# Performance work log

Hardware: AMD Instinct MI355X
Metric: run time of the kernel (lower is better)

Reference implementation:

```python
import jax, jax.numpy as jnp
import numpy as np

KEEP_ID, DEL_ID, PAD_ID, STOP_ID, ANNO_ID = 1, 2, 0, 102, 103
V, E, H = 21128, 768, 768
B, T = 8, 256
S = T + 1  # org/simp length; S = T+1 guarantees counters never go out of range


def setup_inputs() -> dict:
    key = jax.random.key(0)
    ks = jax.random.split(key, 16)
    def p(i, shape, scale):
        return jax.random.normal(ks[i], shape, jnp.float32) * scale
    return {
        "input_edits": jax.random.randint(ks[0], (B, T), 0, V),
        "org_ids": jax.random.randint(ks[1], (B, S), 0, V),
        "simp_sent": jax.random.randint(ks[2], (B, S), 0, V),
        "h0": jax.random.normal(ks[3], (B, H), jnp.float32),
        "c0": jax.random.normal(ks[4], (B, H), jnp.float32),
        "encoder_outputs_org": jax.random.normal(ks[5], (B, S, E), jnp.float32),
        "emb": p(6, (V, E), 0.02),
        "Wih_e": p(7, (4 * H, E), 0.03), "Whh_e": p(8, (4 * H, H), 0.03), "b_e": jnp.zeros((4 * H,), jnp.float32),
        "Wih_w": p(9, (4 * H, E), 0.03), "Whh_w": p(10, (4 * H, H), 0.03), "b_w": jnp.zeros((4 * H,), jnp.float32),
        "W_attn": p(11, (H, H), 0.03),
        "W_align": p(12, (H, E), 0.03),
        "W_mlp": p(13, (E, 4 * H), 0.03), "b_mlp": jnp.zeros((E,), jnp.float32),
        "W_out": p(14, (V, E), 0.02), "b_out": jnp.zeros((V,), jnp.float32),
    }


def lstm(x, h0, c0, Wih, Whh, b):
    # x: [B,T,E]; single-layer batch_first LSTM, torch gate order (i,f,g,o)
    def step(carry, xt):
        h, c = carry
        g = xt @ Wih.T + h @ Whh.T + b
        i, f, gg, o = jnp.split(g, 4, axis=-1)
        c2 = jax.nn.sigmoid(f) * c + jax.nn.sigmoid(i) * jnp.tanh(gg)
        h2 = jax.nn.sigmoid(o) * jnp.tanh(c2)
        return (h2, c2), h2
    (hT, cT), hs = jax.lax.scan(step, (h0, c0), jnp.swapaxes(x, 0, 1))
    return jnp.swapaxes(hs, 0, 1), hT, cT


def reference(input_edits, org_ids, simp_sent, h0, c0, encoder_outputs_org,
              emb, Wih_e, Whh_e, b_e, Wih_w, Whh_w, b_w,
              W_attn, W_align, W_mlp, b_mlp, W_out, b_out):
    bsz, nsteps = input_edits.shape
    enc = jnp.tanh(encoder_outputs_org @ W_align.T)            # [B,S,H]
    out_edits, hT, cT = lstm(emb[input_edits], h0, c0, Wih_e, Whh_e, b_e)  # [B,T,H]
    out_words, _, _ = lstm(emb[simp_sent], h0, c0, Wih_w, Whh_w, b_w)      # [B,S,H]

    key = out_edits @ W_attn.T                                  # [B,T,H]
    attn = jax.nn.softmax(jnp.einsum('bth,bsh->bts', key, enc), axis=-1)
    ctx = jnp.einsum('bts,bsh->bth', attn, enc)                 # [B,T,H]

    # counter recurrence (pre-update counters are used for the gathers at step t)
    gold = jnp.swapaxes(input_edits[:, 1:], 0, 1)               # [T-1, B]
    bidx = jnp.arange(bsz)

    def cstep(carry, a):
        kd, ki, an = carry
        kd2 = kd + ((a == KEEP_ID) | (a == DEL_ID)).astype(kd.dtype)
        not_special = (a != DEL_ID) & (a != STOP_ID) & (a != PAD_ID)
        ki2 = ki + not_special.astype(ki.dtype)
        is_ins = not_special & (a != KEEP_ID)
        next_is_anno = org_ids[bidx, an + 1] == ANNO_ID
        an2 = jnp.where(is_ins & next_is_anno, an + 1, jnp.maximum(kd2, an))
        return (kd2, ki2, an2), (ki, an)

    z = jnp.zeros((bsz,), jnp.int32)
    _, (ki_seq, an_seq) = jax.lax.scan(cstep, (z, z, z), gold)
    ki_bt = jnp.swapaxes(ki_seq, 0, 1)                          # [B,T-1]
    an_bt = jnp.swapaxes(an_seq, 0, 1)                          # [B,T-1]

    c = jnp.take_along_axis(enc, an_bt[:, :, None], axis=1)        # [B,T-1,H]
    c_word = jnp.take_along_axis(out_words, ki_bt[:, :, None], axis=1)  # [B,T-1,H]

    Tm1 = nsteps - 1
    feat = jnp.concatenate([out_edits[:, :Tm1], ctx[:, :Tm1], c, c_word], axis=-1)  # [B,T-1,4H]
    mlp = jnp.tanh(feat @ W_mlp.T + b_mlp)                      # [B,T-1,E]
    logp = jax.nn.log_softmax(mlp @ W_out.T + b_out, axis=-1)   # [B,T-1,V]
    return logp, hT, cT
```

## Files before the change

kernel.cpp:

```cpp
#include <hip/hip_runtime.h>
#include <hip/hip_bf16.h>

typedef short s16x8 __attribute__((ext_vector_type(8)));
typedef float f32x4 __attribute__((ext_vector_type(4)));
typedef unsigned short u16;
typedef unsigned short u16x4 __attribute__((ext_vector_type(4)));
typedef unsigned long long u64;
typedef unsigned long long u64x2 __attribute__((ext_vector_type(2)));

__device__ __forceinline__ u16 f2bf(float f) {
  __hip_bfloat16 h = __float2bfloat16(f);
  u16 u;
  __builtin_memcpy(&u, &h, sizeof(u));
  return u;
}
__device__ __forceinline__ float bf2f(u16 u) {
  unsigned int x = ((unsigned int)u) << 16;
  float f;
  __builtin_memcpy(&f, &x, 4);
  return f;
}

__device__ __forceinline__ unsigned int a_ld32(const unsigned int* p) {
  return __hip_atomic_load(p, __ATOMIC_RELAXED, __HIP_MEMORY_SCOPE_AGENT);
}
__device__ __forceinline__ u64 a_ld64(const u64* p) {
  return __hip_atomic_load(p, __ATOMIC_RELAXED, __HIP_MEMORY_SCOPE_AGENT);
}
__device__ __forceinline__ void a_st32(unsigned int* p, unsigned int v) {
  __hip_atomic_store(p, v, __ATOMIC_RELAXED, __HIP_MEMORY_SCOPE_AGENT);
}

__device__ __forceinline__ void gload16(const void* g, void* l) {
  __builtin_amdgcn_global_load_lds(
      (const __attribute__((address_space(1))) unsigned int*)g,
      (__attribute__((address_space(3))) unsigned int*)l, 16, 0, 0);
}

template<int CBF16, int GATHER, int TANHA, int BIAS>
__global__ __launch_bounds__(256) void gemm_bt(
    const u16* __restrict__ A, const u16* __restrict__ B,
    const float* __restrict__ bias, void* __restrict__ Cv,
    const int* __restrict__ ids,
    int M, int N, int K, int lda, int ldb, int ldc,
    long sAz, long sBz, long sCz, int rpb, long cbs)
{
  __shared__ u16 sA[4096];
  __shared__ u16 sB[4096];
  const int tid = threadIdx.x;
  const int z = blockIdx.z;
  const int m0 = blockIdx.y * 128, n0 = blockIdx.x * 128;
  const u16* Ab = A + z * sAz;
  const u16* Bb = B + z * sBz;
  const int w = tid >> 6, lane = tid & 63;
  const int wr = w >> 1, wc = w & 1;
  const int lr = lane & 15, lk = lane >> 4;
  f32x4 acc[4][4] = {};
  const int e0 = tid * 8, e1 = e0 + 2048;
  const int r0 = e0 >> 5, c0 = e0 & 31;
  const int r1 = e1 >> 5, c1 = e1 & 31;
  long arow0, arow1;
  if (GATHER) {
    int i0 = m0 + r0; if (i0 >= M) i0 = M - 1;
    int i1 = m0 + r1; if (i1 >= M) i1 = M - 1;
    arow0 = (long)ids[i0] * lda;
    arow1 = (long)ids[i1] * lda;
  } else {
    arow0 = (long)(m0 + r0) * lda;
    arow1 = (long)(m0 + r1) * lda;
  }
  const long brow0 = (long)(n0 + r0) * ldb;
  const long brow1 = (long)(n0 + r1) * ldb;
  char* sAc = (char*)sA;
  char* sBc = (char*)sB;
  const size_t cb = (size_t)w * 1024;
  for (int kt = 0; kt < K; kt += 32) {
    __syncthreads();
    gload16(Ab + arow0 + kt + c0, sAc + cb);
    gload16(Ab + arow1 + kt + c1, sAc + 4096 + cb);
    gload16(Bb + brow0 + kt + c0, sBc + cb);
    gload16(Bb + brow1 + kt + c1, sBc + 4096 + cb);
    __syncthreads();
    s16x8 af[4], bf[4];
#pragma unroll
    for (int i = 0; i < 4; i++) {
      af[i] = *(const s16x8*)&sA[(wr*64 + i*16 + lr)*32 + lk*8];
      bf[i] = *(const s16x8*)&sB[(wc*64 + i*16 + lr)*32 + lk*8];
    }
#pragma unroll
    for (int mi = 0; mi < 4; mi++)
#pragma unroll
      for (int ni = 0; ni < 4; ni++)
        acc[mi][ni] = __builtin_amdgcn_mfma_f32_16x16x32_bf16(af[mi], bf[ni], acc[mi][ni], 0, 0, 0);
  }
#pragma unroll
  for (int mi = 0; mi < 4; mi++) {
#pragma unroll
    for (int ni = 0; ni < 4; ni++) {
#pragma unroll
      for (int r = 0; r < 4; r++) {
        int gm = m0 + wr*64 + mi*16 + lk*4 + r;
        int gn = n0 + wc*64 + ni*16 + lr;
        if (gm < M && gn < N) {
          float v = acc[mi][ni][r];
          if (BIAS) v += bias[gn];
          if (TANHA) v = tanhf(v);
          long ci = z * sCz + (long)(gm / rpb) * cbs + (long)(gm % rpb) * ldc + gn;
          if (CBF16) ((u16*)Cv)[ci] = f2bf(v);
          else       ((float*)Cv)[ci] = v;
        }
      }
    }
  }
}

__global__ __launch_bounds__(256) void cast_all(
    const float* __restrict__ emb, u16* __restrict__ emb_bf,
    const float* __restrict__ Wout, u16* __restrict__ Wout_bf,
    const float* __restrict__ Wihe, u16* __restrict__ Wihe_bf,
    const float* __restrict__ Wihw, u16* __restrict__ Wihw_bf,
    const float* __restrict__ Wmlp, u16* __restrict__ Wmlp_bf,
    const float* __restrict__ Walign, u16* __restrict__ Walign_bf,
    const float* __restrict__ Wattn, u16* __restrict__ Wattn_bf,
    const float* __restrict__ encoder, u16* __restrict__ encd_bf)
{
  int r = blockIdx.x;
  const float* src; u16* dst; int srows, cols;
  if (r < 21128)                    { src=emb;    dst=emb_bf;    srows=21128; cols=768; }
  else if ((r -= 21128) < 21248)    { src=Wout;   dst=Wout_bf;   srows=21128; cols=768; }
  else if ((r -= 21248) < 3072)     { src=Wihe;   dst=Wihe_bf;   srows=3072;  cols=768; }
  else if ((r -= 3072) < 3072)      { src=Wihw;   dst=Wihw_bf;   srows=3072;  cols=768; }
  else if ((r -= 3072) < 768)       { src=Wmlp;   dst=Wmlp_bf;   srows=768;   cols=3072; }
  else if ((r -= 768) < 768)        { src=Walign; dst=Walign_bf; srows=768;   cols=768; }
  else if ((r -= 768) < 768)        { src=Wattn;  dst=Wattn_bf;  srows=768;   cols=768; }
  else { r -= 768;                    src=encoder; dst=encd_bf;  srows=2056;  cols=768; }
  for (int c = threadIdx.x; c < cols; c += 256) {
    float v = (r < srows) ? src[(long)r * cols + c] : 0.f;
    dst[(long)r * cols + c] = f2bf(v);
  }
}

__global__ void counters_k(const int* __restrict__ input_edits,
                           const int* __restrict__ org_ids,
                           int* __restrict__ ki_bt, int* __restrict__ an_bt,
                           unsigned int* __restrict__ tags)
{
  int b = threadIdx.x;
  for (int i = b; i < 128; i += 64) tags[i] = 0;
  if (b >= 8) return;
  int kd = 0, ki = 0, an = 0;
  for (int t = 0; t < 255; t++) {
    int a = input_edits[b * 256 + t + 1];
    ki_bt[b * 255 + t] = ki;
    an_bt[b * 255 + t] = an;
    int kd2 = kd + ((a == 1) || (a == 2) ? 1 : 0);
    int ns = (a != 2) && (a != 102) && (a != 0);
    int ki2 = ki + (ns ? 1 : 0);
    int is_ins = ns && (a != 1);
    int nia = (org_ids[b * 257 + an + 1] == 103);
    int mx = (kd2 > an) ? kd2 : an;
    int an2 = (is_ins && nia) ? (an + 1) : mx;
    kd = kd2; ki = ki2; an = an2;
  }
}

__global__ __launch_bounds__(256, 1) void lstm_persist(
    const float* __restrict__ Whh_e, const float* __restrict__ Whh_w,
    const float* __restrict__ xW_e, const float* __restrict__ xW_w,
    const float* __restrict__ h0, const float* __restrict__ c0,
    u16* __restrict__ hglob, unsigned int* __restrict__ tags,
    u16* __restrict__ out_e, u16* __restrict__ out_w,
    float* __restrict__ out_tail)
{
  const int wg = blockIdx.x;
  const int l = wg / 24, grp = wg % 24;
  const int u0 = grp * 32;
  const int tid = threadIdx.x;
  const int w = tid >> 6, lane = tid & 63;
  const int c16 = lane & 15, half = lane >> 4;
  const int uh = w >> 1, g0 = (w & 1) * 2;

  __shared__ u16 ldsh[12288];
  __shared__ float Gbuf[16][4][2][16];

  s16x8 wfrag[2][24];
  {
    const float* Wbase = l ? Whh_w : Whh_e;
#pragma unroll
    for (int g = 0; g < 2; g++) {
      const float* Wsrc = Wbase + (long)((g0 + g) * 768 + u0 + uh * 16 + c16) * 768 + half * 8;
#pragma unroll
      for (int s = 0; s < 24; s++) {
        float4 f0 = *(const float4*)(Wsrc + s * 32);
        float4 f1 = *(const float4*)(Wsrc + s * 32 + 4);
        s16x8 v;
        v[0]=f2bf(f0.x); v[1]=f2bf(f0.y); v[2]=f2bf(f0.z); v[3]=f2bf(f0.w);
        v[4]=f2bf(f1.x); v[5]=f2bf(f1.y); v[6]=f2bf(f1.z); v[7]=f2bf(f1.w);
        wfrag[g][s] = v;
      }
    }
  }

  const int ub = tid >> 4, j2 = (tid & 15) * 2;
  const int uA = u0 + j2;
  float creg0 = 0.f, creg1 = 0.f;
  if (tid < 128) {
    creg0 = c0[ub * 768 + uA];
    creg1 = c0[ub * 768 + uA + 1];
  }

  u16* hg = hglob + l * 24576;
  unsigned int* tg = tags + l * 64;
  const int swA = uA ^ ((ub & 7) << 3);

  if (tid < 128) {
    float v0 = h0[ub * 768 + uA], v1 = h0[ub * 768 + uA + 1];
    u16 h0a = f2bf(v0), h0b = f2bf(v1);
    u16 l0a = f2bf(v0 - bf2f(h0a)), l0b = f2bf(v1 - bf2f(h0b));
    a_st32((unsigned int*)&hg[ub * 768 + swA],
           (unsigned int)h0a | ((unsigned int)h0b << 16));
    a_st32((unsigned int*)&hg[(ub + 8) * 768 + swA],
           (unsigned int)l0a | ((unsigned int)l0b << 16));
  }
  __syncthreads();
  if (tid == 0) a_st32(&tg[grp], 1u);

  const int trow = l ? 257 : 256;
  const float* xrb = (l ? xW_w : xW_e) + ((long)ub * trow) * 3072 + uA;
  u16* outp = (l ? out_w : out_e) + (long)ub * 256 * 768 + uA;
  float2 xq0, xq1, xq2, xq3;
  if (tid < 128) {
    xq0 = *(const float2*)&xrb[0];
    xq1 = *(const float2*)&xrb[768];
    xq2 = *(const float2*)&xrb[1536];
    xq3 = *(const float2*)&xrb[2304];
  }

  for (int t = 0; t < 256; t++) {
    float2 nx0, nx1, nx2, nx3;
    if (tid < 128) {
      const float* xn = xrb + (long)(t + 1) * 3072;
      nx0 = *(const float2*)&xn[0];
      nx1 = *(const float2*)&xn[768];
      nx2 = *(const float2*)&xn[1536];
      nx3 = *(const float2*)&xn[2304];
    }

    {
      const unsigned int tgt = (unsigned int)(t + 1);
      const unsigned int* tp = tg + (t & 1) * 32;
      const bool need = (lane < 24) && (lane != grp);
      while (true) {
        unsigned int v = need ? a_ld32(&tp[lane]) : tgt;
        if (!__any(v < tgt)) break;
        __builtin_amdgcn_s_sleep(1);
      }
      asm volatile("" ::: "memory");
    }

    {
      const u64* hs8 = (const u64*)(hg + (t & 1) * 12288);
#pragma unroll
      for (int i = 0; i < 6; i++) {
        const int idx = i * 256 + tid;
        u64 a = a_ld64(&hs8[idx * 2 + 0]);
        u64 b = a_ld64(&hs8[idx * 2 + 1]);
        u64x2 vv; vv[0] = a; vv[1] = b;
        *(u64x2*)&ldsh[idx * 8] = vv;
      }
    }
    __syncthreads();

    f32x4 acc0 = {}, acc1 = {};
#pragma unroll
    for (int s = 0; s < 24; s++) {
      const int off = (c16 * 768 + s * 32 + half * 8) ^ ((c16 & 7) << 3);
      s16x8 a = *(const s16x8*)&ldsh[off];
      acc0 = __builtin_amdgcn_mfma_f32_16x16x32_bf16(a, wfrag[0][s], acc0, 0, 0, 0);
      acc1 = __builtin_amdgcn_mfma_f32_16x16x32_bf16(a, wfrag[1][s], acc1, 0, 0, 0);
    }
#pragma unroll
    for (int r = 0; r < 4; r++) {
      Gbuf[half * 4 + r][g0 + 0][uh][c16] = acc0[r];
      Gbuf[half * 4 + r][g0 + 1][uh][c16] = acc1[r];
    }
    __syncthreads();

    if (tid < 128) {
      const int uh0 = j2 >> 4, uc0 = j2 & 15;
      const int uc1 = (j2 + 1) & 15;
      float gi0 = Gbuf[ub][0][uh0][uc0] + Gbuf[ub + 8][0][uh0][uc0] + xq0.x;
      float gf0 = Gbuf[ub][1][uh0][uc0] + Gbuf[ub + 8][1][uh0][uc0] + xq1.x;
      float gg0 = Gbuf[ub][2][uh0][uc0] + Gbuf[ub + 8][2][uh0][uc0] + xq2.x;
      float go0 = Gbuf[ub][3][uh0][uc0] + Gbuf[ub + 8][3][uh0][uc0] + xq3.x;
      float gi1 = Gbuf[ub][0][uh0][uc1] + Gbuf[ub + 8][0][uh0][uc1] + xq0.y;
      float gf1 = Gbuf[ub][1][uh0][uc1] + Gbuf[ub + 8][1][uh0][uc1] + xq1.y;
      float gg1 = Gbuf[ub][2][uh0][uc1] + Gbuf[ub + 8][2][uh0][uc1] + xq2.y;
      float go1 = Gbuf[ub][3][uh0][uc1] + Gbuf[ub + 8][3][uh0][uc1] + xq3.y;
      float si0 = 1.f / (1.f + expf(-gi0)), si1 = 1.f / (1.f + expf(-gi1));
      float sf0 = 1.f / (1.f + expf(-gf0)), sf1 = 1.f / (1.f + expf(-gf1));
      float so0 = 1.f / (1.f + expf(-go0)), so1 = 1.f / (1.f + expf(-go1));
      float c20 = sf0 * creg0 + si0 * tanhf(gg0);
      float c21 = sf1 * creg1 + si1 * tanhf(gg1);
      float h20 = so0 * tanhf(c20);
      float h21 = so1 * tanhf(c21);
      creg0 = c20; creg1 = c21;
      u16 hiA = f2bf(h20), hiB = f2bf(h21);
      u16 loA = f2bf(h20 - bf2f(hiA)), loB = f2bf(h21 - bf2f(hiB));
      unsigned int hip = (unsigned int)hiA | ((unsigned int)hiB << 16);
      unsigned int lop = (unsigned int)loA | ((unsigned int)loB << 16);
      u16* hb = hg + ((t + 1) & 1) * 12288;
      a_st32((unsigned int*)&hb[ub * 768 + swA], hip);
      a_st32((unsigned int*)&hb[(ub + 8) * 768 + swA], lop);
      *(unsigned int*)&outp[(long)t * 768] = hip;
      if (l == 0 && t == 255) {
        *(float2*)&out_tail[43101120 + ub * 768 + uA] = make_float2(h20, h21);
        *(float2*)&out_tail[43107264 + ub * 768 + uA] = make_float2(c20, c21);
      }
      xq0 = nx0; xq1 = nx1; xq2 = nx2; xq3 = nx3;
    }
    __syncthreads();
    if (tid == 0)
      a_st32(&tg[((t + 1) & 1) * 32 + grp], (unsigned int)(t + 2));
  }
}

__global__ __launch_bounds__(256) void softmax_k(
    const float* __restrict__ scores, u16* __restrict__ attn)
{
  const int row = blockIdx.x;
  const float* src = scores + (long)row * 288;
  u16* dst = attn + (long)row * 288;
  const int tid = threadIdx.x;
  float v0 = (tid < 257) ? src[tid] : -1e30f;
  float v1 = (tid + 256 < 257) ? src[tid + 256] : -1e30f;
  float mx = fmaxf(v0, v1);
  for (int o = 32; o; o >>= 1) mx = fmaxf(mx, __shfl_xor(mx, o));
  __shared__ float sm[4];
  __shared__ float ss[4];
  if ((tid & 63) == 0) sm[tid >> 6] = mx;
  __syncthreads();
  mx = fmaxf(fmaxf(sm[0], sm[1]), fmaxf(sm[2], sm[3]));
  float e0 = (tid < 257) ? expf(v0 - mx) : 0.f;
  float e1 = (tid + 256 < 257) ? expf(v1 - mx) : 0.f;
  float s = e0 + e1;
  for (int o = 32; o; o >>= 1) s += __shfl_xor(s, o);
  if ((tid & 63) == 0) ss[tid >> 6] = s;
  __syncthreads();
  s = ss[0] + ss[1] + ss[2] + ss[3];
  float inv = 1.f / s;
  dst[tid] = f2bf(e0 * inv);
  if (tid + 256 < 288) dst[tid + 256] = f2bf(e1 * inv);
}

__global__ __launch_bounds__(256) void transpose_enc(
    const u16* __restrict__ enc, u16* __restrict__ encT)
{
  __shared__ u16 tile[32][33];
  const int b = blockIdx.z, h0 = blockIdx.y * 32, s0 = blockIdx.x * 32;
  const int tx = threadIdx.x & 31, ty = threadIdx.x >> 5;
#pragma unroll
  for (int i = 0; i < 32; i += 8) {
    int s = s0 + ty + i;
    u16 v = (s < 257) ? enc[((long)b * 384 + s) * 768 + h0 + tx] : (u16)0;
    tile[ty + i][tx] = v;
  }
  __syncthreads();
#pragma unroll
  for (int i = 0; i < 32; i += 8) {
    int h = h0 + ty + i;
    encT[((long)b * 768 + h) * 288 + s0 + tx] = tile[tx][ty + i];
  }
}

__global__ __launch_bounds__(256) void feat_k(
    const u16* __restrict__ oute, const u16* __restrict__ ctx,
    const u16* __restrict__ encb, const u16* __restrict__ outw,
    const int* __restrict__ ki_bt, const int* __restrict__ an_bt,
    u16* __restrict__ feat)
{
  int q = blockIdx.x * 256 + threadIdx.x;
  int m = q / 768, qq = q - m * 768;
  int seg = qq / 192, off = (qq - seg * 192) * 4;
  u16x4 v = {0, 0, 0, 0};
  if (m < 2040) {
    int b = m / 255, t = m - b * 255;
    const u16* src;
    if (seg == 0)      src = oute + ((long)(b * 256 + t)) * 768 + off;
    else if (seg == 1) src = ctx  + ((long)(b * 256 + t)) * 768 + off;
    else if (seg == 2) src = encb + ((long)(b * 384 + an_bt[m])) * 768 + off;
    else               src = outw + ((long)(b * 256 + ki_bt[m])) * 768 + off;
    v = *(const u16x4*)src;
  }
  *(u16x4*)(feat + (long)q * 4) = v;
}

__global__ __launch_bounds__(256) void logsoftmax_k(float* __restrict__ logits)
{
  const int m = blockIdx.x;
  float* row = logits + (long)m * 21128;
  const int tid = threadIdx.x;
  float mx = -1e30f, sm = 0.f;
  for (int i = tid * 4; i < 21128; i += 1024) {
    float4 v = *(const float4*)(row + i);
    float m4 = fmaxf(fmaxf(v.x, v.y), fmaxf(v.z, v.w));
    if (m4 > mx) { sm *= expf(mx - m4); mx = m4; }
    sm += expf(v.x - mx) + expf(v.y - mx) + expf(v.z - mx) + expf(v.w - mx);
  }
  for (int o = 32; o; o >>= 1) {
    float mo = __shfl_xor(mx, o), so = __shfl_xor(sm, o);
    float nm = fmaxf(mx, mo);
    sm = sm * expf(mx - nm) + so * expf(mo - nm);
    mx = nm;
  }
  __shared__ float wm[4], wsum[4];
  __shared__ float srs;
  if ((tid & 63) == 0) { wm[tid >> 6] = mx; wsum[tid >> 6] = sm; }
  __syncthreads();
  if (tid == 0) {
    float M = wm[0], S = wsum[0];
    for (int i = 1; i < 4; i++) {
      float nm = fmaxf(M, wm[i]);
      S = S * expf(M - nm) + wsum[i] * expf(wm[i] - nm);
      M = nm;
    }
    srs = M + logf(S);
  }
  __syncthreads();
  const float rs = srs;
  for (int i = tid * 4; i < 21128; i += 1024) {
    float4 v = *(const float4*)(row + i);
    v.x -= rs; v.y -= rs; v.z -= rs; v.w -= rs;
    *(float4*)(row + i) = v;
  }
}

extern "C" void kernel_launch(void* const* d_in, const int* in_sizes, int n_in,
                              void* d_out, int out_size, void* d_ws, size_t ws_size,
                              hipStream_t stream) {
  (void)in_sizes; (void)n_in; (void)out_size; (void)ws_size;
  const int*   input_edits = (const int*)d_in[0];
  const int*   org_ids     = (const int*)d_in[1];
  const int*   simp_sent   = (const int*)d_in[2];
  const float* h0      = (const float*)d_in[3];
  const float* c0      = (const float*)d_in[4];
  const float* encoder = (const float*)d_in[5];
  const float* emb     = (const float*)d_in[6];
  const float* Wih_e   = (const float*)d_in[7];
  const float* Whh_e   = (const float*)d_in[8];
  const float* b_e     = (const float*)d_in[9];
  const float* Wih_w   = (const float*)d_in[10];
  const float* Whh_w   = (const float*)d_in[11];
  const float* b_w     = (const float*)d_in[12];
  const float* W_attn  = (const float*)d_in[13];
  const float* W_align = (const float*)d_in[14];
  const float* W_mlp   = (const float*)d_in[15];
  const float* b_mlp   = (const float*)d_in[16];
  const float* W_out   = (const float*)d_in[17];
  const float* b_out   = (const float*)d_in[18];

  float* out = (float*)d_out;
  float* xW_e = out;
  float* xW_w = out + 2048L * 3072;
  u16* emb_bf  = (u16*)(out + 2048L * 3072 + 2056L * 3072);
  u16* encd_bf = emb_bf + 21128L * 768;
  u16* feat_bf = encd_bf + 2176L * 768;

  char* p = (char*)d_ws;
  auto alloc = [&](size_t bytes) -> char* {
    char* r = p; p += (bytes + 255) & ~(size_t)255; return r;
  };
  u16* Wout_bf   = (u16*)alloc(21248L * 768 * 2);
  u16* Wihe_bf   = (u16*)alloc(3072L * 768 * 2);
  u16* Wihw_bf   = (u16*)alloc(3072L * 768 * 2);
  u16* Wmlp_bf   = (u16*)alloc(768L * 3072 * 2);
  u16* Walign_bf = (u16*)alloc(768L * 768 * 2);
  u16* Wattn_bf  = (u16*)alloc(768L * 768 * 2);
  u16* enc_bf    = (u16*)alloc(8L * 384 * 768 * 2);
  u16* encT_bf   = (u16*)alloc(8L * 768 * 288 * 2);
  u16* oute_bf   = (u16*)alloc(2048L * 768 * 2);
  u16* outw_bf   = (u16*)alloc(2048L * 768 * 2);
  u16* key_bf    = (u16*)alloc(2048L * 768 * 2);
  u16* attn_bf   = (u16*)alloc(8L * 256 * 288 * 2);
  u16* ctx_bf    = (u16*)alloc(2048L * 768 * 2);
  u16* mlp_bf    = (u16*)alloc(2048L * 768 * 2);
  float* scores  = (float*)alloc(8L * 256 * 288 * 4);
  u16* hglob     = (u16*)alloc(2L * 2 * 12288 * 2);
  unsigned int* tags = (unsigned int*)alloc(128 * 4);
  int* ki_bt     = (int*)alloc(2040 * 4);
  int* an_bt     = (int*)alloc(2040 * 4);

  dim3 blk(256);
  const int BIGR = 1 << 30;

  cast_all<<<53000, blk, 0, stream>>>(emb, emb_bf, W_out, Wout_bf,
                                      Wih_e, Wihe_bf, Wih_w, Wihw_bf,
                                      W_mlp, Wmlp_bf, W_align, Walign_bf,
                                      W_attn, Wattn_bf, encoder, encd_bf);
  counters_k<<<1, 64, 0, stream>>>(input_edits, org_ids, ki_bt, an_bt, tags);

  gemm_bt<1, 0, 1, 0><<<dim3(6, 17, 1), blk, 0, stream>>>(
      encd_bf, Walign_bf, nullptr, enc_bf, nullptr,
      2056, 768, 768, 768, 768, 768, 0, 0, 0, 257, 294912L);

  gemm_bt<0, 1, 0, 1><<<dim3(24, 16, 1), blk, 0, stream>>>(
      emb_bf, Wihe_bf, b_e, xW_e, input_edits,
      2048, 3072, 768, 768, 768, 3072, 0, 0, 0, BIGR, 0);
  gemm_bt<0, 1, 0, 1><<<dim3(24, 17, 1), blk, 0, stream>>>(
      emb_bf, Wihw_bf, b_w, xW_w, simp_sent,
      2056, 3072, 768, 768, 768, 3072, 0, 0, 0, BIGR, 0);

  lstm_persist<<<48, blk, 0, stream>>>(
      Whh_e, Whh_w, xW_e, xW_w, h0, c0, hglob, tags,
      oute_bf, outw_bf, out);

  gemm_bt<1, 0, 0, 0><<<dim3(6, 16, 1), blk, 0, stream>>>(
      oute_bf, Wattn_bf, nullptr, key_bf, nullptr,
      2048, 768, 768, 768, 768, 768, 0, 0, 0, BIGR, 0);
  gemm_bt<0, 0, 0, 0><<<dim3(3, 2, 8), blk, 0, stream>>>(
      key_bf, enc_bf, nullptr, scores, nullptr,
      256, 257, 768, 768, 768, 288, 196608L, 294912L, 73728L, BIGR, 0);
  softmax_k<<<2048, blk, 0, stream>>>(scores, attn_bf);
  transpose_enc<<<dim3(9, 24, 8), blk, 0, stream>>>(enc_bf, encT_bf);
  gemm_bt<1, 0, 0, 0><<<dim3(6, 2, 8), blk, 0, stream>>>(
      attn_bf, encT_bf, nullptr, ctx_bf, nullptr,
      256, 768, 288, 288, 288, 768, 73728L, 221184L, 196608L, BIGR, 0);

  feat_k<<<6144, blk, 0, stream>>>(oute_bf, ctx_bf, enc_bf, outw_bf,
                                   ki_bt, an_bt, feat_bf);
  gemm_bt<1, 0, 1, 1><<<dim3(6, 16, 1), blk, 0, stream>>>(
      feat_bf, Wmlp_bf, b_mlp, mlp_bf, nullptr,
      2040, 768, 3072, 3072, 3072, 768, 0, 0, 0, BIGR, 0);
  gemm_bt<0, 0, 0, 1><<<dim3(166, 16, 1), blk, 0, stream>>>(
      mlp_bf, Wout_bf, b_out, out, nullptr,
      2040, 21128, 768, 768, 768, 21128, 0, 0, 0, BIGR, 0);

  logsoftmax_k<<<2040, blk, 0, stream>>>(out);
}
```

Measured before the change: 1.729 ms.

## Restructure LSTM step to drop LDS staging and barriers, merge small launches

Measured after the change: 3.439 ms. 1.99x slower.

```diff
diff --git a/kernel.cpp b/kernel.cpp
--- a/kernel.cpp
+++ b/kernel.cpp
@@ -6,7 +6,6 @@
 typedef unsigned short u16;
 typedef unsigned short u16x4 __attribute__((ext_vector_type(4)));
 typedef unsigned long long u64;
-typedef unsigned long long u64x2 __attribute__((ext_vector_type(2)));
 
 __device__ __forceinline__ u16 f2bf(float f) {
   __hip_bfloat16 h = __float2bfloat16(f);
@@ -43,12 +42,18 @@
     const float* __restrict__ bias, void* __restrict__ Cv,
     const int* __restrict__ ids,
     int M, int N, int K, int lda, int ldb, int ldc,
-    long sAz, long sBz, long sCz, int rpb, long cbs)
+    long sAz, long sBz, long sCz, int rpb, long cbs,
+    const int* __restrict__ ids2, const float* __restrict__ bias2, int dM)
 {
   __shared__ u16 sA[4096];
   __shared__ u16 sB[4096];
   const int tid = threadIdx.x;
   const int z = blockIdx.z;
+  if (z) {
+    if (dM) M += dM;
+    if (ids2) ids = ids2;
+    if (bias2) bias = bias2;
+  }
   const int m0 = blockIdx.y * 128, n0 = blockIdx.x * 128;
   const u16* Ab = A + z * sAz;
   const u16* Bb = B + z * sBz;
@@ -122,9 +127,32 @@
     const float* __restrict__ Wmlp, u16* __restrict__ Wmlp_bf,
     const float* __restrict__ Walign, u16* __restrict__ Walign_bf,
     const float* __restrict__ Wattn, u16* __restrict__ Wattn_bf,
-    const float* __restrict__ encoder, u16* __restrict__ encd_bf)
+    const float* __restrict__ encoder, u16* __restrict__ encd_bf,
+    const int* __restrict__ input_edits, const int* __restrict__ org_ids,
+    int* __restrict__ ki_bt, int* __restrict__ an_bt,
+    unsigned int* __restrict__ tags)
 {
   int r = blockIdx.x;
+  if (r == 53000) {
+    int b = threadIdx.x;
+    if (b < 128) tags[b] = 0;
+    if (b >= 8) return;
+    int kd = 0, ki = 0, an = 0;
+    for (int t = 0; t < 255; t++) {
+      int a = input_edits[b * 256 + t + 1];
+      ki_bt[b * 255 + t] = ki;
+      an_bt[b * 255 + t] = an;
+      int kd2 = kd + ((a == 1) || (a == 2) ? 1 : 0);
+      int ns = (a != 2) && (a != 102) && (a != 0);
+      int ki2 = ki + (ns ? 1 : 0);
+      int is_ins = ns && (a != 1);
+      int nia = (org_ids[b * 257 + an + 1] == 103);
+      int mx = (kd2 > an) ? kd2 : an;
+      int an2 = (is_ins && nia) ? (an + 1) : mx;
+      kd = kd2; ki = ki2; an = an2;
+    }
+    return;
+  }
   const float* src; u16* dst; int srows, cols;
   if (r < 21128)                    { src=emb;    dst=emb_bf;    srows=21128; cols=768; }
   else if ((r -= 21128) < 21248)    { src=Wout;   dst=Wout_bf;   srows=21128; cols=768; }
@@ -140,30 +168,6 @@
   }
 }
 
-__global__ void counters_k(const int* __restrict__ input_edits,
-                           const int* __restrict__ org_ids,
-                           int* __restrict__ ki_bt, int* __restrict__ an_bt,
-                           unsigned int* __restrict__ tags)
-{
-  int b = threadIdx.x;
-  for (int i = b; i < 128; i += 64) tags[i] = 0;
-  if (b >= 8) return;
-  int kd = 0, ki = 0, an = 0;
-  for (int t = 0; t < 255; t++) {
-    int a = input_edits[b * 256 + t + 1];
-    ki_bt[b * 255 + t] = ki;
-    an_bt[b * 255 + t] = an;
-    int kd2 = kd + ((a == 1) || (a == 2) ? 1 : 0);
-    int ns = (a != 2) && (a != 102) && (a != 0);
-    int ki2 = ki + (ns ? 1 : 0);
-    int is_ins = ns && (a != 1);
-    int nia = (org_ids[b * 257 + an + 1] == 103);
-    int mx = (kd2 > an) ? kd2 : an;
-    int an2 = (is_ins && nia) ? (an + 1) : mx;
-    kd = kd2; ki = ki2; an = an2;
-  }
-}
-
 __global__ __launch_bounds__(256, 1) void lstm_persist(
     const float* __restrict__ Whh_e, const float* __restrict__ Whh_w,
     const float* __restrict__ xW_e, const float* __restrict__ xW_w,
@@ -177,18 +181,16 @@
   const int u0 = grp * 32;
   const int tid = threadIdx.x;
   const int w = tid >> 6, lane = tid & 63;
-  const int c16 = lane & 15, half = lane >> 4;
-  const int uh = w >> 1, g0 = (w & 1) * 2;
-
-  __shared__ u16 ldsh[12288];
-  __shared__ float Gbuf[16][4][2][16];
+  const int c16 = lane & 15, q = lane >> 4;
+  const int gate = c16 & 3, ulo = c16 >> 2;
+  const int ubase = u0 + w * 8 + ulo;
 
   s16x8 wfrag[2][24];
   {
     const float* Wbase = l ? Whh_w : Whh_e;
 #pragma unroll
-    for (int g = 0; g < 2; g++) {
-      const float* Wsrc = Wbase + (long)((g0 + g) * 768 + u0 + uh * 16 + c16) * 768 + half * 8;
+    for (int a = 0; a < 2; a++) {
+      const float* Wsrc = Wbase + (long)(gate * 768 + ubase + a * 4) * 768 + q * 8;
 #pragma unroll
       for (int s = 0; s < 24; s++) {
         float4 f0 = *(const float4*)(Wsrc + s * 32);
@@ -196,54 +198,60 @@
         s16x8 v;
         v[0]=f2bf(f0.x); v[1]=f2bf(f0.y); v[2]=f2bf(f0.z); v[3]=f2bf(f0.w);
         v[4]=f2bf(f1.x); v[5]=f2bf(f1.y); v[6]=f2bf(f1.z); v[7]=f2bf(f1.w);
-        wfrag[g][s] = v;
+        wfrag[a][s] = v;
       }
     }
-  }
-
-  const int ub = tid >> 4, j2 = (tid & 15) * 2;
-  const int uA = u0 + j2;
-  float creg0 = 0.f, creg1 = 0.f;
-  if (tid < 128) {
-    creg0 = c0[ub * 768 + uA];
-    creg1 = c0[ub * 768 + uA + 1];
   }
 
   u16* hg = hglob + l * 24576;
   unsigned int* tg = tags + l * 64;
-  const int swA = uA ^ ((ub & 7) << 3);
 
   if (tid < 128) {
-    float v0 = h0[ub * 768 + uA], v1 = h0[ub * 768 + uA + 1];
+    int ub = tid >> 4, col = u0 + (tid & 15) * 2;
+    float v0 = h0[ub * 768 + col], v1 = h0[ub * 768 + col + 1];
     u16 h0a = f2bf(v0), h0b = f2bf(v1);
     u16 l0a = f2bf(v0 - bf2f(h0a)), l0b = f2bf(v1 - bf2f(h0b));
-    a_st32((unsigned int*)&hg[ub * 768 + swA],
+    a_st32((unsigned int*)&hg[ub * 768 + col],
            (unsigned int)h0a | ((unsigned int)h0b << 16));
-    a_st32((unsigned int*)&hg[(ub + 8) * 768 + swA],
+    a_st32((unsigned int*)&hg[(ub + 8) * 768 + col],
            (unsigned int)l0a | ((unsigned int)l0b << 16));
   }
   __syncthreads();
   if (tid == 0) a_st32(&tg[grp], 1u);
 
+  float creg[2][4];
+  if (q < 2) {
+#pragma unroll
+    for (int a = 0; a < 2; a++)
+#pragma unroll
+      for (int r = 0; r < 4; r++)
+        creg[a][r] = c0[(q * 4 + r) * 768 + ubase + a * 4];
+  }
   const int trow = l ? 257 : 256;
-  const float* xrb = (l ? xW_w : xW_e) + ((long)ub * trow) * 3072 + uA;
-  u16* outp = (l ? out_w : out_e) + (long)ub * 256 * 768 + uA;
-  float2 xq0, xq1, xq2, xq3;
-  if (tid < 128) {
-    xq0 = *(const float2*)&xrb[0];
-    xq1 = *(const float2*)&xrb[768];
-    xq2 = *(const float2*)&xrb[1536];
-    xq3 = *(const float2*)&xrb[2304];
-  }
+  const float* xb = (l ? xW_w : xW_e) + gate * 768 + ubase;
+  u16* oub = l ? out_w : out_e;
+
+  float xq[2][4] = {};
+  if (q < 2) {
+#pragma unroll
+    for (int a = 0; a < 2; a++)
+#pragma unroll
+      for (int r = 0; r < 4; r++)
+        xq[a][r] = xb[(long)(q * 4 + r) * trow * 3072 + a * 4];
+  }
+
+  const int abase = c16 * 192 + q * 2;
+  const bool stlane = (q < 2) && (gate == 0) && ((c16 & 4) == 0);
+  const int colp = u0 + w * 8 + ((c16 >> 2) & 2);
 
   for (int t = 0; t < 256; t++) {
-    float2 nx0, nx1, nx2, nx3;
-    if (tid < 128) {
-      const float* xn = xrb + (long)(t + 1) * 3072;
-      nx0 = *(const float2*)&xn[0];
-      nx1 = *(const float2*)&xn[768];
-      nx2 = *(const float2*)&xn[1536];
-      nx3 = *(const float2*)&xn[2304];
+    float nx[2][4] = {};
+    if (q < 2 && t < 255) {
+#pragma unroll
+      for (int a = 0; a < 2; a++)
+#pragma unroll
+        for (int r = 0; r < 4; r++)
+          nx[a][r] = xb[((long)(q * 4 + r) * trow + t + 1) * 3072 + a * 4];
     }
 
     {
@@ -258,67 +266,74 @@
       asm volatile("" ::: "memory");
     }
 
-    {
-      const u64* hs8 = (const u64*)(hg + (t & 1) * 12288);
-#pragma unroll
-      for (int i = 0; i < 6; i++) {
-        const int idx = i * 256 + tid;
-        u64 a = a_ld64(&hs8[idx * 2 + 0]);
-        u64 b = a_ld64(&hs8[idx * 2 + 1]);
-        u64x2 vv; vv[0] = a; vv[1] = b;
-        *(u64x2*)&ldsh[idx * 8] = vv;
-      }
-    }
-    __syncthreads();
+    const u64* hb8 = (const u64*)(hg + (t & 1) * 12288);
+    s16x8 af[24];
+#pragma unroll
+    for (int s = 0; s < 24; s++) {
+      u64 arr[2];
+      arr[0] = a_ld64(hb8 + abase + s * 8);
+      arr[1] = a_ld64(hb8 + abase + s * 8 + 1);
+      __builtin_memcpy(&af[s], arr, 16);
+    }
 
     f32x4 acc0 = {}, acc1 = {};
 #pragma unroll
     for (int s = 0; s < 24; s++) {
-      const int off = (c16 * 768 + s * 32 + half * 8) ^ ((c16 & 7) << 3);
-      s16x8 a = *(const s16x8*)&ldsh[off];
-      acc0 = __builtin_amdgcn_mfma_f32_16x16x32_bf16(a, wfrag[0][s], acc0, 0, 0, 0);
-      acc1 = __builtin_amdgcn_mfma_f32_16x16x32_bf16(a, wfrag[1][s], acc1, 0, 0, 0);
-    }
-#pragma unroll
-    for (int r = 0; r < 4; r++) {
-      Gbuf[half * 4 + r][g0 + 0][uh][c16] = acc0[r];
-      Gbuf[half * 4 + r][g0 + 1][uh][c16] = acc1[r];
-    }
-    __syncthreads();
-
-    if (tid < 128) {
-      const int uh0 = j2 >> 4, uc0 = j2 & 15;
-      const int uc1 = (j2 + 1) & 15;
-      float gi0 = Gbuf[ub][0][uh0][uc0] + Gbuf[ub + 8][0][uh0][uc0] + xq0.x;
-      float gf0 = Gbuf[ub][1][uh0][uc0] + Gbuf[ub + 8][1][uh0][uc0] + xq1.x;
-      float gg0 = Gbuf[ub][2][uh0][uc0] + Gbuf[ub + 8][2][uh0][uc0] + xq2.x;
-      float go0 = Gbuf[ub][3][uh0][uc0] + Gbuf[ub + 8][3][uh0][uc0] + xq3.x;
-      float gi1 = Gbuf[ub][0][uh0][uc1] + Gbuf[ub + 8][0][uh0][uc1] + xq0.y;
-      float gf1 = Gbuf[ub][1][uh0][uc1] + Gbuf[ub + 8][1][uh0][uc1] + xq1.y;
-      float gg1 = Gbuf[ub][2][uh0][uc1] + Gbuf[ub + 8][2][uh0][uc1] + xq2.y;
-      float go1 = Gbuf[ub][3][uh0][uc1] + Gbuf[ub + 8][3][uh0][uc1] + xq3.y;
-      float si0 = 1.f / (1.f + expf(-gi0)), si1 = 1.f / (1.f + expf(-gi1));
-      float sf0 = 1.f / (1.f + expf(-gf0)), sf1 = 1.f / (1.f + expf(-gf1));
-      float so0 = 1.f / (1.f + expf(-go0)), so1 = 1.f / (1.f + expf(-go1));
-      float c20 = sf0 * creg0 + si0 * tanhf(gg0);
-      float c21 = sf1 * creg1 + si1 * tanhf(gg1);
-      float h20 = so0 * tanhf(c20);
-      float h21 = so1 * tanhf(c21);
-      creg0 = c20; creg1 = c21;
-      u16 hiA = f2bf(h20), hiB = f2bf(h21);
-      u16 loA = f2bf(h20 - bf2f(hiA)), loB = f2bf(h21 - bf2f(hiB));
-      unsigned int hip = (unsigned int)hiA | ((unsigned int)hiB << 16);
-      unsigned int lop = (unsigned int)loA | ((unsigned int)loB << 16);
-      u16* hb = hg + ((t + 1) & 1) * 12288;
-      a_st32((unsigned int*)&hb[ub * 768 + swA], hip);
-      a_st32((unsigned int*)&hb[(ub + 8) * 768 + swA], lop);
-      *(unsigned int*)&outp[(long)t * 768] = hip;
-      if (l == 0 && t == 255) {
-        *(float2*)&out_tail[43101120 + ub * 768 + uA] = make_float2(h20, h21);
-        *(float2*)&out_tail[43107264 + ub * 768 + uA] = make_float2(c20, c21);
-      }
-      xq0 = nx0; xq1 = nx1; xq2 = nx2; xq3 = nx3;
-    }
+      acc0 = __builtin_amdgcn_mfma_f32_16x16x32_bf16(af[s], wfrag[0][s], acc0, 0, 0, 0);
+      acc1 = __builtin_amdgcn_mfma_f32_16x16x32_bf16(af[s], wfrag[1][s], acc1, 0, 0, 0);
+    }
+
+    u16* hb = hg + ((t + 1) & 1) * 12288;
+    const bool lastt = (l == 0) && (t == 255);
+
+#define UPD(ACCV, A)                                                          \
+    {                                                                         \
+      _Pragma("unroll")                                                       \
+      for (int r = 0; r < 4; r++) {                                           \
+        float s0 = (ACCV)[r] + __shfl_xor((ACCV)[r], 32);                     \
+        if (q < 2) s0 += xq[A][r];                                            \
+        float t1v = __shfl_xor(s0, 1);                                        \
+        float t2v = __shfl_xor(s0, 2);                                        \
+        float t3v = __shfl_xor(s0, 3);                                        \
+        int m1 = gate ^ 1, m2 = gate ^ 2, m3 = gate ^ 3;                      \
+        float gi = gate == 0 ? s0 : gate == 1 ? t1v : gate == 2 ? t2v : t3v;  \
+        float gf = m1 == 0 ? s0 : m1 == 1 ? t1v : m1 == 2 ? t2v : t3v;        \
+        float gg = m2 == 0 ? s0 : m2 == 1 ? t1v : m2 == 2 ? t2v : t3v;        \
+        float go = m3 == 0 ? s0 : m3 == 1 ? t1v : m3 == 2 ? t2v : t3v;        \
+        float si = 1.f / (1.f + expf(-gi));                                   \
+        float sf = 1.f / (1.f + expf(-gf));                                   \
+        float so = 1.f / (1.f + expf(-go));                                   \
+        float c2 = sf * creg[A][r] + si * tanhf(gg);                          \
+        float h2 = so * tanhf(c2);                                            \
+        creg[A][r] = c2;                                                      \
+        u16 hu = f2bf(h2), lu = f2bf(h2 - bf2f(hu));                          \
+        unsigned int hi32 = hu, lo32 = lu;                                    \
+        unsigned int nhi = __shfl_xor(hi32, 4), nlo = __shfl_xor(lo32, 4);    \
+        if (stlane) {                                                         \
+          int b = q * 4 + r, col = colp + (A) * 4;                            \
+          a_st32((unsigned int*)&hb[b * 768 + col], hi32 | (nhi << 16));      \
+          a_st32((unsigned int*)&hb[(b + 8) * 768 + col], lo32 | (nlo << 16));\
+          *(unsigned int*)&oub[((long)(b * 256 + t)) * 768 + col] =           \
+              hi32 | (nhi << 16);                                             \
+        }                                                                     \
+        if (lastt && q < 2 && gate == 0) {                                    \
+          int b = q * 4 + r, u = ubase + (A) * 4;                             \
+          out_tail[43101120 + b * 768 + u] = h2;                              \
+          out_tail[43107264 + b * 768 + u] = c2;                              \
+        }                                                                     \
+      }                                                                       \
+    }
+
+    UPD(acc0, 0)
+    UPD(acc1, 1)
+#undef UPD
+
+#pragma unroll
+    for (int a = 0; a < 2; a++)
+#pragma unroll
+      for (int r = 0; r < 4; r++)
+        xq[a][r] = nx[a][r];
+
     __syncthreads();
     if (tid == 0)
       a_st32(&tg[((t + 1) & 1) * 32 + grp], (unsigned int)(t + 2));
@@ -493,22 +508,21 @@
   dim3 blk(256);
   const int BIGR = 1 << 30;
 
-  cast_all<<<53000, blk, 0, stream>>>(emb, emb_bf, W_out, Wout_bf,
+  cast_all<<<53001, blk, 0, stream>>>(emb, emb_bf, W_out, Wout_bf,
                                       Wih_e, Wihe_bf, Wih_w, Wihw_bf,
                                       W_mlp, Wmlp_bf, W_align, Walign_bf,
-                                      W_attn, Wattn_bf, encoder, encd_bf);
-  counters_k<<<1, 64, 0, stream>>>(input_edits, org_ids, ki_bt, an_bt, tags);
+                                      W_attn, Wattn_bf, encoder, encd_bf,
+                                      input_edits, org_ids, ki_bt, an_bt, tags);
 
   gemm_bt<1, 0, 1, 0><<<dim3(6, 17, 1), blk, 0, stream>>>(
       encd_bf, Walign_bf, nullptr, enc_bf, nullptr,
-      2056, 768, 768, 768, 768, 768, 0, 0, 0, 257, 294912L);
-
-  gemm_bt<0, 1, 0, 1><<<dim3(24, 16, 1), blk, 0, stream>>>(
+      2056, 768, 768, 768, 768, 768, 0, 0, 0, 257, 294912L,
+      nullptr, nullptr, 0);
+
+  gemm_bt<0, 1, 0, 1><<<dim3(24, 17, 2), blk, 0, stream>>>(
       emb_bf, Wihe_bf, b_e, xW_e, input_edits,
-      2048, 3072, 768, 768, 768, 3072, 0, 0, 0, BIGR, 0);
-  gemm_bt<0, 1, 0, 1><<<dim3(24, 17, 1), blk, 0, stream>>>(
-      emb_bf, Wihw_bf, b_w, xW_w, simp_sent,
-      2056, 3072, 768, 768, 768, 3072, 0, 0, 0, BIGR, 0);
+      2048, 3072, 768, 768, 768, 3072, 0, 2359296L, 6291456L, BIGR, 0,
+      simp_sent, b_w, 8);
 
   lstm_persist<<<48, blk, 0, stream>>>(
       Whh_e, Whh_w, xW_e, xW_w, h0, c0, hglob, tags,
@@ -516,24 +530,29 @@
 
   gemm_bt<1, 0, 0, 0><<<dim3(6, 16, 1), blk, 0, stream>>>(
       oute_bf, Wattn_bf, nullptr, key_bf, nullptr,
-      2048, 768, 768, 768, 768, 768, 0, 0, 0, BIGR, 0);
+      2048, 768, 768, 768, 768, 768, 0, 0, 0, BIGR, 0,
+      nullptr, nullptr, 0);
   gemm_bt<0, 0, 0, 0><<<dim3(3, 2, 8), blk, 0, stream>>>(
       key_bf, enc_bf, nullptr, scores, nullptr,
-      256, 257, 768, 768, 768, 288, 196608L, 294912L, 73728L, BIGR, 0);
+      256, 257, 768, 768, 768, 288, 196608L, 294912L, 73728L, BIGR, 0,
+      nullptr, nullptr, 0);
   softmax_k<<<2048, blk, 0, stream>>>(scores, attn_bf);
   transpose_enc<<<dim3(9, 24, 8), blk, 0, stream>>>(enc_bf, encT_bf);
   gemm_bt<1, 0, 0, 0><<<dim3(6, 2, 8), blk, 0, stream>>>(
       attn_bf, encT_bf, nullptr, ctx_bf, nullptr,
-      256, 768, 288, 288, 288, 768, 73728L, 221184L, 196608L, BIGR, 0);
+      256, 768, 288, 288, 288, 768, 73728L, 221184L, 196608L, BIGR, 0,
+      nullptr, nullptr, 0);
 
   feat_k<<<6144, blk, 0, stream>>>(oute_bf, ctx_bf, enc_bf, outw_bf,
                                    ki_bt, an_bt, feat_bf);
   gemm_bt<1, 0, 1, 1><<<dim3(6, 16, 1), blk, 0, stream>>>(
       feat_bf, Wmlp_bf, b_mlp, mlp_bf, nullptr,
-      2040, 768, 3072, 3072, 3072, 768, 0, 0, 0, BIGR, 0);
+      2040, 768, 3072, 3072, 3072, 768, 0, 0, 0, BIGR, 0,
+      nullptr, nullptr, 0);
   gemm_bt<0, 0, 0, 1><<<dim3(166, 16, 1), blk, 0, stream>>>(
       mlp_bf, Wout_bf, b_out, out, nullptr,
-      2040, 21128, 768, 768, 768, 21128, 0, 0, 0, BIGR, 0);
+      2040, 21128, 768, 768, 768, 21128, 0, 0, 0, BIGR, 0,
+      nullptr, nullptr, 0);
 
   logsoftmax_k<<<2040, blk, 0, stream>>>(out);
 }
```

## Fold counters into cast kernel, merge input GEMMs, use per-wave LSTM flags

Applied to the files above, without the earlier changes.

Result: slower. 2.175 ms (+25.8%).

```diff
diff --git a/kernel.cpp b/kernel.cpp
--- a/kernel.cpp
+++ b/kernel.cpp
@@ -43,12 +43,18 @@
     const float* __restrict__ bias, void* __restrict__ Cv,
     const int* __restrict__ ids,
     int M, int N, int K, int lda, int ldb, int ldc,
-    long sAz, long sBz, long sCz, int rpb, long cbs)
+    long sAz, long sBz, long sCz, int rpb, long cbs,
+    const int* __restrict__ ids2, const float* __restrict__ bias2, int dM)
 {
   __shared__ u16 sA[4096];
   __shared__ u16 sB[4096];
   const int tid = threadIdx.x;
   const int z = blockIdx.z;
+  if (z) {
+    if (dM) M += dM;
+    if (ids2) ids = ids2;
+    if (bias2) bias = bias2;
+  }
   const int m0 = blockIdx.y * 128, n0 = blockIdx.x * 128;
   const u16* Ab = A + z * sAz;
   const u16* Bb = B + z * sBz;
@@ -122,9 +128,32 @@
     const float* __restrict__ Wmlp, u16* __restrict__ Wmlp_bf,
     const float* __restrict__ Walign, u16* __restrict__ Walign_bf,
     const float* __restrict__ Wattn, u16* __restrict__ Wattn_bf,
-    const float* __restrict__ encoder, u16* __restrict__ encd_bf)
+    const float* __restrict__ encoder, u16* __restrict__ encd_bf,
+    const int* __restrict__ input_edits, const int* __restrict__ org_ids,
+    int* __restrict__ ki_bt, int* __restrict__ an_bt,
+    unsigned int* __restrict__ tags)
 {
   int r = blockIdx.x;
+  if (r == 53000) {
+    int b = threadIdx.x;
+    tags[b] = 0;
+    if (b >= 8) return;
+    int kd = 0, ki = 0, an = 0;
+    for (int t = 0; t < 255; t++) {
+      int a = input_edits[b * 256 + t + 1];
+      ki_bt[b * 255 + t] = ki;
+      an_bt[b * 255 + t] = an;
+      int kd2 = kd + ((a == 1) || (a == 2) ? 1 : 0);
+      int ns = (a != 2) && (a != 102) && (a != 0);
+      int ki2 = ki + (ns ? 1 : 0);
+      int is_ins = ns && (a != 1);
+      int nia = (org_ids[b * 257 + an + 1] == 103);
+      int mx = (kd2 > an) ? kd2 : an;
+      int an2 = (is_ins && nia) ? (an + 1) : mx;
+      kd = kd2; ki = ki2; an = an2;
+    }
+    return;
+  }
   const float* src; u16* dst; int srows, cols;
   if (r < 21128)                    { src=emb;    dst=emb_bf;    srows=21128; cols=768; }
   else if ((r -= 21128) < 21248)    { src=Wout;   dst=Wout_bf;   srows=21128; cols=768; }
@@ -140,30 +169,6 @@
   }
 }
 
-__global__ void counters_k(const int* __restrict__ input_edits,
-                           const int* __restrict__ org_ids,
-                           int* __restrict__ ki_bt, int* __restrict__ an_bt,
-                           unsigned int* __restrict__ tags)
-{
-  int b = threadIdx.x;
-  for (int i = b; i < 128; i += 64) tags[i] = 0;
-  if (b >= 8) return;
-  int kd = 0, ki = 0, an = 0;
-  for (int t = 0; t < 255; t++) {
-    int a = input_edits[b * 256 + t + 1];
-    ki_bt[b * 255 + t] = ki;
-    an_bt[b * 255 + t] = an;
-    int kd2 = kd + ((a == 1) || (a == 2) ? 1 : 0);
-    int ns = (a != 2) && (a != 102) && (a != 0);
-    int ki2 = ki + (ns ? 1 : 0);
-    int is_ins = ns && (a != 1);
-    int nia = (org_ids[b * 257 + an + 1] == 103);
-    int mx = (kd2 > an) ? kd2 : an;
-    int an2 = (is_ins && nia) ? (an + 1) : mx;
-    kd = kd2; ki = ki2; an = an2;
-  }
-}
-
 __global__ __launch_bounds__(256, 1) void lstm_persist(
     const float* __restrict__ Whh_e, const float* __restrict__ Whh_w,
     const float* __restrict__ xW_e, const float* __restrict__ xW_w,
@@ -210,7 +215,7 @@
   }
 
   u16* hg = hglob + l * 24576;
-  unsigned int* tg = tags + l * 64;
+  unsigned int* tg = tags + l * 128;
   const int swA = uA ^ ((ub & 7) << 3);
 
   if (tid < 128) {
@@ -222,8 +227,10 @@
     a_st32((unsigned int*)&hg[(ub + 8) * 768 + swA],
            (unsigned int)l0a | ((unsigned int)l0b << 16));
   }
-  __syncthreads();
-  if (tid == 0) a_st32(&tg[grp], 1u);
+  if (w < 2) {
+    asm volatile("s_waitcnt vmcnt(0)" ::: "memory");
+    if (lane == 0) a_st32(&tg[grp * 2 + w], 1u);
+  }
 
   const int trow = l ? 257 : 256;
   const float* xrb = (l ? xW_w : xW_e) + ((long)ub * trow) * 3072 + uA;
@@ -248,10 +255,9 @@
 
     {
       const unsigned int tgt = (unsigned int)(t + 1);
-      const unsigned int* tp = tg + (t & 1) * 32;
-      const bool need = (lane < 24) && (lane != grp);
+      const unsigned int* tp = tg + (t & 1) * 64;
       while (true) {
-        unsigned int v = need ? a_ld32(&tp[lane]) : tgt;
+        unsigned int v = (lane < 48) ? a_ld32(&tp[lane]) : tgt;
         if (!__any(v < tgt)) break;
         __builtin_amdgcn_s_sleep(1);
       }
@@ -286,6 +292,8 @@
     }
     __syncthreads();
 
+    unsigned int hip = 0;
+    float h20 = 0.f, h21 = 0.f, c20 = 0.f, c21 = 0.f;
     if (tid < 128) {
       const int uh0 = j2 >> 4, uc0 = j2 & 15;
       const int uc1 = (j2 + 1) & 15;
@@ -300,28 +308,34 @@
       float si0 = 1.f / (1.f + expf(-gi0)), si1 = 1.f / (1.f + expf(-gi1));
       float sf0 = 1.f / (1.f + expf(-gf0)), sf1 = 1.f / (1.f + expf(-gf1));
       float so0 = 1.f / (1.f + expf(-go0)), so1 = 1.f / (1.f + expf(-go1));
-      float c20 = sf0 * creg0 + si0 * tanhf(gg0);
-      float c21 = sf1 * creg1 + si1 * tanhf(gg1);
-      float h20 = so0 * tanhf(c20);
-      float h21 = so1 * tanhf(c21);
+      c20 = sf0 * creg0 + si0 * tanhf(gg0);
+      c21 = sf1 * creg1 + si1 * tanhf(gg1);
+      h20 = so0 * tanhf(c20);
+      h21 = so1 * tanhf(c21);
       creg0 = c20; creg1 = c21;
       u16 hiA = f2bf(h20), hiB = f2bf(h21);
       u16 loA = f2bf(h20 - bf2f(hiA)), loB = f2bf(h21 - bf2f(hiB));
-      unsigned int hip = (unsigned int)hiA | ((unsigned int)hiB << 16);
+      hip = (unsigned int)hiA | ((unsigned int)hiB << 16);
       unsigned int lop = (unsigned int)loA | ((unsigned int)loB << 16);
       u16* hb = hg + ((t + 1) & 1) * 12288;
       a_st32((unsigned int*)&hb[ub * 768 + swA], hip);
       a_st32((unsigned int*)&hb[(ub + 8) * 768 + swA], lop);
+      xq0 = nx0; xq1 = nx1; xq2 = nx2; xq3 = nx3;
+    }
+
+    if (w < 2) {
+      asm volatile("s_waitcnt vmcnt(0)" ::: "memory");
+      if (lane == 0)
+        a_st32(&tg[((t + 1) & 1) * 64 + grp * 2 + w], (unsigned int)(t + 2));
+    }
+
+    if (tid < 128) {
       *(unsigned int*)&outp[(long)t * 768] = hip;
       if (l == 0 && t == 255) {
         *(float2*)&out_tail[43101120 + ub * 768 + uA] = make_float2(h20, h21);
         *(float2*)&out_tail[43107264 + ub * 768 + uA] = make_float2(c20, c21);
       }
-      xq0 = nx0; xq1 = nx1; xq2 = nx2; xq3 = nx3;
-    }
-    __syncthreads();
-    if (tid == 0)
-      a_st32(&tg[((t + 1) & 1) * 32 + grp], (unsigned int)(t + 2));
+    }
   }
 }
 
@@ -486,29 +500,28 @@
   u16* mlp_bf    = (u16*)alloc(2048L * 768 * 2);
   float* scores  = (float*)alloc(8L * 256 * 288 * 4);
   u16* hglob     = (u16*)alloc(2L * 2 * 12288 * 2);
-  unsigned int* tags = (unsigned int*)alloc(128 * 4);
+  unsigned int* tags = (unsigned int*)alloc(256 * 4);
   int* ki_bt     = (int*)alloc(2040 * 4);
   int* an_bt     = (int*)alloc(2040 * 4);
 
   dim3 blk(256);
   const int BIGR = 1 << 30;
 
-  cast_all<<<53000, blk, 0, stream>>>(emb, emb_bf, W_out, Wout_bf,
+  cast_all<<<53001, blk, 0, stream>>>(emb, emb_bf, W_out, Wout_bf,
                                       Wih_e, Wihe_bf, Wih_w, Wihw_bf,
                                       W_mlp, Wmlp_bf, W_align, Walign_bf,
-                                      W_attn, Wattn_bf, encoder, encd_bf);
-  counters_k<<<1, 64, 0, stream>>>(input_edits, org_ids, ki_bt, an_bt, tags);
+                                      W_attn, Wattn_bf, encoder, encd_bf,
+                                      input_edits, org_ids, ki_bt, an_bt, tags);
 
   gemm_bt<1, 0, 1, 0><<<dim3(6, 17, 1), blk, 0, stream>>>(
       encd_bf, Walign_bf, nullptr, enc_bf, nullptr,
-      2056, 768, 768, 768, 768, 768, 0, 0, 0, 257, 294912L);
-
-  gemm_bt<0, 1, 0, 1><<<dim3(24, 16, 1), blk, 0, stream>>>(
+      2056, 768, 768, 768, 768, 768, 0, 0, 0, 257, 294912L,
+      nullptr, nullptr, 0);
+
+  gemm_bt<0, 1, 0, 1><<<dim3(24, 17, 2), blk, 0, stream>>>(
       emb_bf, Wihe_bf, b_e, xW_e, input_edits,
-      2048, 3072, 768, 768, 768, 3072, 0, 0, 0, BIGR, 0);
-  gemm_bt<0, 1, 0, 1><<<dim3(24, 17, 1), blk, 0, stream>>>(
-      emb_bf, Wihw_bf, b_w, xW_w, simp_sent,
-      2056, 3072, 768, 768, 768, 3072, 0, 0, 0, BIGR, 0);
+      2048, 3072, 768, 768, 768, 3072, 0, 2359296L, 6291456L, BIGR, 0,
+      simp_sent, b_w, 8);
 
   lstm_persist<<<48, blk, 0, stream>>>(
       Whh_e, Whh_w, xW_e, xW_w, h0, c0, hglob, tags,
@@ -516,24 +529,29 @@
 
   gemm_bt<1, 0, 0, 0><<<dim3(6, 16, 1), blk, 0, stream>>>(
       oute_bf, Wattn_bf, nullptr, key_bf, nullptr,
-      2048, 768, 768, 768, 768, 768, 0, 0, 0, BIGR, 0);
+      2048, 768, 768, 768, 768, 768, 0, 0, 0, BIGR, 0,
+      nullptr, nullptr, 0);
   gemm_bt<0, 0, 0, 0><<<dim3(3, 2, 8), blk, 0, stream>>>(
       key_bf, enc_bf, nullptr, scores, nullptr,
-      256, 257, 768, 768, 768, 288, 196608L, 294912L, 73728L, BIGR, 0);
+      256, 257, 768, 768, 768, 288, 196608L, 294912L, 73728L, BIGR, 0,
+      nullptr, nullptr, 0);
   softmax_k<<<2048, blk, 0, stream>>>(scores, attn_bf);
   transpose_enc<<<dim3(9, 24, 8), blk, 0, stream>>>(enc_bf, encT_bf);
   gemm_bt<1, 0, 0, 0><<<dim3(6, 2, 8), blk, 0, stream>>>(
       attn_bf, encT_bf, nullptr, ctx_bf, nullptr,
-      256, 768, 288, 288, 288, 768, 73728L, 221184L, 196608L, BIGR, 0);
+      256, 768, 288, 288, 288, 768, 73728L, 221184L, 196608L, BIGR, 0,
+      nullptr, nullptr, 0);
 
   feat_k<<<6144, blk, 0, stream>>>(oute_bf, ctx_bf, enc_bf, outw_bf,
                                    ki_bt, an_bt, feat_bf);
   gemm_bt<1, 0, 1, 1><<<dim3(6, 16, 1), blk, 0, stream>>>(
       feat_bf, Wmlp_bf, b_mlp, mlp_bf, nullptr,
-      2040, 768, 3072, 3072, 3072, 768, 0, 0, 0, BIGR, 0);
+      2040, 768, 3072, 3072, 3072, 768, 0, 0, 0, BIGR, 0,
+      nullptr, nullptr, 0);
   gemm_bt<0, 0, 0, 1><<<dim3(166, 16, 1), blk, 0, stream>>>(
       mlp_bf, Wout_bf, b_out, out, nullptr,
-      2040, 21128, 768, 768, 768, 21128, 0, 0, 0, BIGR, 0);
+      2040, 21128, 768, 768, 768, 21128, 0, 0, 0, BIGR, 0,
+      nullptr, nullptr, 0);
 
   logsoftmax_k<<<2040, blk, 0, stream>>>(out);
 }
```
